# Performance work log

Measured on AMD Instinct MI355X. Metric: run time of the kernel, lower is better.

Reference implementation:

```python
import jax, jax.numpy as jnp
import numpy as np

B, S, D, H, MAX_OBJ, N_IMGS = 256, 256, 256, 4, 50, 32


def setup_inputs() -> dict:
    key = jax.random.key(0)
    ks = jax.random.split(key, 8)
    std = 1.0 / np.sqrt(D)
    mk = lambda k: (jax.random.normal(k, (D, D), jnp.float32) * std)
    return {
        "batch_seq": jax.random.normal(ks[0], (B, S, D), jnp.float32),
        "img_ids": jax.random.randint(ks[1], (B,), 0, N_IMGS, jnp.int32),
        "Wq": mk(ks[2]), "Wk": mk(ks[3]), "Wv": mk(ks[4]), "Wo": mk(ks[5]),
        "bq": jnp.zeros((D,), jnp.float32), "bk": jnp.zeros((D,), jnp.float32),
        "bv": jnp.zeros((D,), jnp.float32), "bo": jnp.zeros((D,), jnp.float32),
        "obj_emb": jax.random.normal(ks[6], (MAX_OBJ, D), jnp.float32) * 0.02,
        "scale": jnp.ones((1,), jnp.float32) * 0.2,
    }


def reference(batch_seq, img_ids, Wq, Wk, Wv, Wo, bq, bk, bv, bo, obj_emb, scale):
    Bn, Sn, Dn = batch_seq.shape
    dh = Dn // H
    idx = jnp.arange(Bn)
    same = img_ids[:, None] == img_ids[None, :]          # (B, B) group membership
    rank = jnp.sum(same & (idx[None, :] < idx[:, None]), axis=1)  # position within group
    gsize = jnp.sum(same, axis=1)                         # group size per item

    # enhanced features: add rank-indexed object embedding (broadcast over seq)
    enh = batch_seq + scale * obj_emb[rank][:, None, :]   # (B, S, D)

    # MHA over the seq dimension, batched over B (eval mode, no dropout)
    q = (enh @ Wq + bq).reshape(Bn, Sn, H, dh)
    k = (enh @ Wk + bk).reshape(Bn, Sn, H, dh)
    v = (enh @ Wv + bv).reshape(Bn, Sn, H, dh)
    scores = jnp.einsum("bqhd,bkhd->bhqk", q, k) / float(np.sqrt(dh))
    attn = jax.nn.softmax(scores, axis=-1)
    ctx = jnp.einsum("bhqk,bkhd->bqhd", attn, v).reshape(Bn, Sn, Dn)
    att_out = ctx @ Wo + bo

    # residual; items in singleton groups are passed through unchanged
    return jnp.where((gsize > 1)[:, None, None], batch_seq + att_out, batch_seq)
```

## Files before the change

### kernel.cpp

```cpp
#include <hip/hip_runtime.h>

typedef __bf16 bf16x8 __attribute__((ext_vector_type(8)));
typedef float f32x4 __attribute__((ext_vector_type(4)));
typedef ushort u16x8 __attribute__((ext_vector_type(8)));

__device__ __forceinline__ float bf2f(ushort u) {
    union { unsigned int i; float f; } v; v.i = ((unsigned int)u) << 16; return v.f;
}
__device__ __forceinline__ ushort f2bf(float f) {
    union { float f; unsigned int i; } v; v.f = f;
    unsigned int i = v.i;
    return (ushort)((i + 0x7FFFu + ((i >> 16) & 1u)) >> 16);
}
__device__ __forceinline__ unsigned int addmul_bf2(unsigned int xs, unsigned int es, float sc) {
    float f0 = bf2f((ushort)(xs & 0xffffu)) + sc * bf2f((ushort)(es & 0xffffu));
    float f1 = bf2f((ushort)(xs >> 16))     + sc * bf2f((ushort)(es >> 16));
    return (unsigned int)f2bf(f0) | (((unsigned int)f2bf(f1)) << 16);
}

__global__ __launch_bounds__(256) void sniff_kernel(
    const unsigned int* __restrict__ bs_words, int* __restrict__ flag)
{
    const int t = threadIdx.x;
    int hit = 0;
    for (int i = 0; i < 64; ++i) {
        unsigned int w = bs_words[t * 64 + i];
        unsigned int e0 = (w >> 7)  & 0xffu;
        unsigned int e1 = (w >> 23) & 0xffu;
        if (e0 > 150u || e1 > 150u) hit = 1;
    }
    __shared__ int s;
    if (t == 0) s = 0;
    __syncthreads();
    if (hit) atomicOr(&s, 1);
    __syncthreads();
    if (t == 0) *flag = s;
}

__global__ __launch_bounds__(256) void prep_kernel(
    const int* __restrict__ flag,
    const void* __restrict__ Wq, const void* __restrict__ Wk,
    const void* __restrict__ Wv, const void* __restrict__ Wo,
    const void* __restrict__ c0, const void* __restrict__ c1,
    const void* __restrict__ c2, const void* __restrict__ c3,
    const void* __restrict__ c4, const void* __restrict__ scale_in,
    int* __restrict__ rank, int* __restrict__ gsize,
    ushort* __restrict__ Wqkv_t, ushort* __restrict__ Wo_t,
    float* __restrict__ bqkv_f, float* __restrict__ bo_f,
    float* __restrict__ scale_f)
{
    const int blk = blockIdx.x;
    const int t = threadIdx.x;
    const bool is_f32 = (*flag != 0);
    if (blk < 256) {
        const int k = blk;
        ushort q, kk, vv, oo;
        if (is_f32) {
            q  = f2bf(((const float*)Wq)[k * 256 + t]);
            kk = f2bf(((const float*)Wk)[k * 256 + t]);
            vv = f2bf(((const float*)Wv)[k * 256 + t]);
            oo = f2bf(((const float*)Wo)[k * 256 + t]);
        } else {
            q  = ((const ushort*)Wq)[k * 256 + t];
            kk = ((const ushort*)Wk)[k * 256 + t];
            vv = ((const ushort*)Wv)[k * 256 + t];
            oo = ((const ushort*)Wo)[k * 256 + t];
        }
        Wqkv_t[(size_t)t * 256 + k]         = q;
        Wqkv_t[(size_t)(256 + t) * 256 + k] = kk;
        Wqkv_t[(size_t)(512 + t) * 256 + k] = vv;
        Wo_t[(size_t)t * 256 + k]           = oo;
    } else {
        const void* cands[5] = {c0, c1, c2, c3, c4};
        __shared__ int cstat[5];
        if (t < 5) cstat[t] = 0;
        __syncthreads();
        #pragma unroll
        for (int c = 0; c < 5; ++c) {
            unsigned int wv = ((const unsigned int*)cands[c])[t];
            int fl = ((wv != 0u) ? 1 : 0) | ((wv >= 32u) ? 2 : 0);
            if (fl) atomicOr(&cstat[c], fl);
        }
        __syncthreads();
        int sel = 0;
        #pragma unroll
        for (int c = 4; c >= 0; --c)
            if (cstat[c] == 1) sel = c;
        const int* ids = (const int*)cands[sel];
        int bp[4];
        { int n = 0;
          #pragma unroll
          for (int c = 0; c < 5; ++c) if (c != sel) bp[n++] = c; }

        const int b = t;
        const int my = ids[b];
        int r = 0, g = 0;
        for (int j = 0; j < 256; ++j) {
            bool same = (ids[j] == my);
            r += (same && (j < b)) ? 1 : 0;
            g += same ? 1 : 0;
        }
        rank[b]  = (r > 49) ? 49 : r;
        gsize[b] = g;

        float vq, vk, vv2, vo2;
        if (is_f32) {
            vq  = ((const float*)cands[bp[0]])[t];
            vk  = ((const float*)cands[bp[1]])[t];
            vv2 = ((const float*)cands[bp[2]])[t];
            vo2 = ((const float*)cands[bp[3]])[t];
            if (t == 0) *scale_f = ((const float*)scale_in)[0];
        } else {
            vq  = bf2f(((const ushort*)cands[bp[0]])[t]);
            vk  = bf2f(((const ushort*)cands[bp[1]])[t]);
            vv2 = bf2f(((const ushort*)cands[bp[2]])[t]);
            vo2 = bf2f(((const ushort*)cands[bp[3]])[t]);
            if (t == 0) *scale_f = bf2f(((const ushort*)scale_in)[0]);
        }
        bqkv_f[t]       = vq;
        bqkv_f[256 + t] = vk;
        bqkv_f[512 + t] = vv2;
        bo_f[t]         = vo2;
    }
}

__global__ __launch_bounds__(256) void enh_kernel(
    const int* __restrict__ flag,
    const void* __restrict__ bs, const void* __restrict__ obj_emb,
    const float* __restrict__ scale_f, const int* __restrict__ rank,
    ushort* __restrict__ enh)
{
    const int idx = blockIdx.x * 256 + threadIdx.x;
    const int e0 = idx * 8;
    const int b = e0 >> 16;
    const int col = e0 & 255;
    const int rk = rank[b];
    const float sc = *scale_f;
    if (*flag != 0) {
        const float* bsf = (const float*)bs + e0;
        const float* ef  = (const float*)obj_emb + rk * 256 + col;
        float4 x0 = *(const float4*)bsf, x1 = *(const float4*)(bsf + 4);
        float4 ev0 = *(const float4*)ef, ev1 = *(const float4*)(ef + 4);
        u16x8 o;
        o[0] = f2bf(x0.x + sc * ev0.x); o[1] = f2bf(x0.y + sc * ev0.y);
        o[2] = f2bf(x0.z + sc * ev0.z); o[3] = f2bf(x0.w + sc * ev0.w);
        o[4] = f2bf(x1.x + sc * ev1.x); o[5] = f2bf(x1.y + sc * ev1.y);
        o[6] = f2bf(x1.z + sc * ev1.z); o[7] = f2bf(x1.w + sc * ev1.w);
        *(u16x8*)(enh + e0) = o;
    } else {
        uint4 x = *(const uint4*)((const ushort*)bs + e0);
        uint4 e = *(const uint4*)((const ushort*)obj_emb + rk * 256 + col);
        uint4 o;
        o.x = addmul_bf2(x.x, e.x, sc);
        o.y = addmul_bf2(x.y, e.y, sc);
        o.z = addmul_bf2(x.z, e.z, sc);
        o.w = addmul_bf2(x.w, e.w, sc);
        *(uint4*)(enh + e0) = o;
    }
}

__global__ __launch_bounds__(256, 2) void qkv_kernel(
    const ushort* __restrict__ enh, const ushort* __restrict__ Wqkv_t,
    const float* __restrict__ bqkv_f,
    ushort* __restrict__ Qg, ushort* __restrict__ Kg, ushort* __restrict__ Vt)
{
    __shared__ __attribute__((aligned(16))) ushort A_lds[64 * 32];
    __shared__ __attribute__((aligned(16))) ushort B_lds[256 * 32];
    __shared__ __attribute__((aligned(16))) ushort Tw[4][64 * 72];

    const int m0 = blockIdx.x * 64;
    const int seg = blockIdx.y;
    const int n0 = seg * 256;
    const int b  = m0 >> 8;
    const int tid = threadIdx.x;
    const int w = tid >> 6, l = tid & 63, quad = l >> 4, l15 = l & 15;

    f32x4 acc[4][4];
    #pragma unroll
    for (int i = 0; i < 4; ++i)
        #pragma unroll
        for (int j = 0; j < 4; ++j) { f32x4 z = {0.f,0.f,0.f,0.f}; acc[i][j] = z; }

    const int arow = tid >> 2, ako = (tid & 3) * 8;
    for (int k0 = 0; k0 < 256; k0 += 32) {
        *(uint4*)&A_lds[arow * 32 + ako] =
            *(const uint4*)(enh + (((size_t)(m0 + arow)) << 8) + k0 + ako);
        #pragma unroll
        for (int i = 0; i < 4; ++i) {
            int f = tid + i * 256;
            int n = f >> 2, ko = (f & 3) * 8;
            *(uint4*)&B_lds[n * 32 + ko] =
                *(const uint4*)(Wqkv_t + (((size_t)(n0 + n)) << 8) + k0 + ko);
        }
        __syncthreads();
        bf16x8 a[4], bb[4];
        #pragma unroll
        for (int mt = 0; mt < 4; ++mt)
            a[mt] = *(const bf16x8*)&A_lds[(mt * 16 + l15) * 32 + quad * 8];
        #pragma unroll
        for (int nt = 0; nt < 4; ++nt)
            bb[nt] = *(const bf16x8*)&B_lds[(w * 64 + nt * 16 + l15) * 32 + quad * 8];
        #pragma unroll
        for (int mt = 0; mt < 4; ++mt)
            #pragma unroll
            for (int nt = 0; nt < 4; ++nt)
                acc[mt][nt] = __builtin_amdgcn_mfma_f32_16x16x32_bf16(
                    a[mt], bb[nt], acc[mt][nt], 0, 0, 0);
        __syncthreads();
    }

    if (seg < 2) {
        const float qs = (seg == 0) ? 0.125f : 1.0f;
        #pragma unroll
        for (int nt = 0; nt < 4; ++nt) {
            const float bias = bqkv_f[seg * 256 + w * 64 + nt * 16 + l15];
            #pragma unroll
            for (int mt = 0; mt < 4; ++mt)
                #pragma unroll
                for (int r = 0; r < 4; ++r)
                    Tw[w][(mt * 16 + quad * 4 + r) * 72 + nt * 16 + l15] =
                        f2bf((acc[mt][nt][r] + bias) * qs);
        }
        ushort* dst = (seg == 0) ? Qg : Kg;
        const size_t bh = (size_t)(b * 4 + w);
        const int sb = m0 & 255;
        #pragma unroll
        for (int i = 0; i < 8; ++i) {
            const int chunk = i * 64 + l;
            const int row = chunk >> 3, dch = chunk & 7;
            u16x8 v = *(const u16x8*)&Tw[w][row * 72 + dch * 8];
            *(u16x8*)(dst + (bh * 256 + sb + row) * 64 + dch * 8) = v;
        }
    } else {
        #pragma unroll
        for (int nt = 0; nt < 4; ++nt) {
            const int n_g = n0 + w * 64 + nt * 16 + l15;
            const int within = n_g & 255;
            const int h = within >> 6, d = within & 63;
            const float bias = bqkv_f[n_g];
            const size_t bh = (size_t)(b * 4 + h);
            #pragma unroll
            for (int mt = 0; mt < 4; ++mt) {
                const int sbase = (m0 & 255) + mt * 16 + quad * 4;
                ushort pk[4];
                #pragma unroll
                for (int r = 0; r < 4; ++r) pk[r] = f2bf(acc[mt][nt][r] + bias);
                *(ushort4*)(Vt + (bh * 64 + d) * 256 + sbase) =
                    make_ushort4(pk[0], pk[1], pk[2], pk[3]);
            }
        }
    }
}

__global__ __launch_bounds__(256, 2) void attn_kernel(
    const ushort* __restrict__ Qg, const ushort* __restrict__ Kg,
    const ushort* __restrict__ Vt, ushort* __restrict__ ctx)
{
    __shared__ __attribute__((aligned(16))) ushort Pl[4][64 * 72];
    const int bh = blockIdx.x;
    const int b = bh >> 2, h = bh & 3;
    const int tid = threadIdx.x;
    const int w = tid >> 6, l = tid & 63, quad = l >> 4, l15 = l & 15;

    const ushort* Qb = Qg + (size_t)bh * 256 * 64;
    const ushort* Kb = Kg + (size_t)bh * 256 * 64;
    const ushort* Vb = Vt + (size_t)bh * 64 * 256;

    bf16x8 qf[4][2];
    #pragma unroll
    for (int mt = 0; mt < 4; ++mt)
        #pragma unroll
        for (int ks = 0; ks < 2; ++ks) {
            int s = w * 64 + mt * 16 + l15;
            qf[mt][ks] = *(const bf16x8*)(Qb + (size_t)s * 64 + ks * 32 + quad * 8);
        }

    f32x4 O[4][4];
    float lsum[4][4];
    #pragma unroll
    for (int mt = 0; mt < 4; ++mt) {
        #pragma unroll
        for (int dt = 0; dt < 4; ++dt) { f32x4 z = {0.f,0.f,0.f,0.f}; O[mt][dt] = z; }
        #pragma unroll
        for (int r = 0; r < 4; ++r) lsum[mt][r] = 0.f;
    }

    for (int c = 0; c < 4; ++c) {
        bf16x8 vf[2][4];
        #pragma unroll
        for (int ks = 0; ks < 2; ++ks)
            #pragma unroll
            for (int dt = 0; dt < 4; ++dt)
                vf[ks][dt] = *(const bf16x8*)(Vb + (size_t)(dt * 16 + l15) * 256 +
                                              c * 64 + ks * 32 + quad * 8);

        f32x4 sacc[4][4];
        #pragma unroll
        for (int mt = 0; mt < 4; ++mt)
            #pragma unroll
            for (int nt = 0; nt < 4; ++nt) { f32x4 z = {0.f,0.f,0.f,0.f}; sacc[mt][nt] = z; }
        #pragma unroll
        for (int ks = 0; ks < 2; ++ks) {
            bf16x8 kf[4];
            #pragma unroll
            for (int nt = 0; nt < 4; ++nt) {
                int key = c * 64 + nt * 16 + l15;
                kf[nt] = *(const bf16x8*)(Kb + (size_t)key * 64 + ks * 32 + quad * 8);
            }
            #pragma unroll
            for (int mt = 0; mt < 4; ++mt)
                #pragma unroll
                for (int nt = 0; nt < 4; ++nt)
                    sacc[mt][nt] = __builtin_amdgcn_mfma_f32_16x16x32_bf16(
                        qf[mt][ks], kf[nt], sacc[mt][nt], 0, 0, 0);
        }

        #pragma unroll
        for (int mt = 0; mt < 4; ++mt)
            #pragma unroll
            for (int nt = 0; nt < 4; ++nt)
                #pragma unroll
                for (int r = 0; r < 4; ++r) {
                    float p = __expf(sacc[mt][nt][r]);
                    lsum[mt][r] += p;
                    Pl[w][(mt * 16 + quad * 4 + r) * 72 + nt * 16 + l15] = f2bf(p);
                }

        #pragma unroll
        for (int ks = 0; ks < 2; ++ks) {
            bf16x8 pf[4];
            #pragma unroll
            for (int mt = 0; mt < 4; ++mt)
                pf[mt] = *(const bf16x8*)&Pl[w][(mt * 16 + l15) * 72 + ks * 32 + quad * 8];
            #pragma unroll
            for (int mt = 0; mt < 4; ++mt)
                #pragma unroll
                for (int dt = 0; dt < 4; ++dt)
                    O[mt][dt] = __builtin_amdgcn_mfma_f32_16x16x32_bf16(
                        pf[mt], vf[ks][dt], O[mt][dt], 0, 0, 0);
        }
    }

    float linv[4][4];
    #pragma unroll
    for (int mt = 0; mt < 4; ++mt)
        #pragma unroll
        for (int r = 0; r < 4; ++r) {
            float v = lsum[mt][r];
            v += __shfl_xor(v, 1);
            v += __shfl_xor(v, 2);
            v += __shfl_xor(v, 4);
            v += __shfl_xor(v, 8);
            linv[mt][r] = 1.0f / v;
        }

    #pragma unroll
    for (int mt = 0; mt < 4; ++mt)
        #pragma unroll
        for (int r = 0; r < 4; ++r) {
            #pragma unroll
            for (int dt = 0; dt < 4; ++dt)
                Pl[w][(mt * 16 + quad * 4 + r) * 72 + dt * 16 + l15] =
                    f2bf(O[mt][dt][r] * linv[mt][r]);
        }
    #pragma unroll
    for (int i = 0; i < 8; ++i) {
        const int chunk = i * 64 + l;
        const int row = chunk >> 3, dch = chunk & 7;
        u16x8 v = *(const u16x8*)&Pl[w][row * 72 + dch * 8];
        *(u16x8*)(ctx + ((size_t)(b * 256 + w * 64 + row)) * 256 + h * 64 + dch * 8) = v;
    }
}

__global__ __launch_bounds__(256, 2) void out_kernel(
    const int* __restrict__ flag,
    const ushort* __restrict__ ctx, const ushort* __restrict__ Wo_t,
    const float* __restrict__ bo_f, const void* __restrict__ bs,
    const int* __restrict__ gsize, void* __restrict__ outv)
{
    __shared__ __attribute__((aligned(16))) ushort A_lds[64 * 32];
    __shared__ __attribute__((aligned(16))) ushort B_lds[256 * 32];
    __shared__ __attribute__((aligned(16))) float  Tf[4][16 * 68];

    const int m0 = blockIdx.x * 64;
    const int tid = threadIdx.x;
    const int w = tid >> 6, l = tid & 63, quad = l >> 4, l15 = l & 15;
    const int b = m0 >> 8;
    const bool pass = (gsize[b] <= 1);
    const bool is_f32 = (*flag != 0);

    f32x4 acc[4][4];
    #pragma unroll
    for (int i = 0; i < 4; ++i)
        #pragma unroll
        for (int j = 0; j < 4; ++j) { f32x4 z = {0.f,0.f,0.f,0.f}; acc[i][j] = z; }

    const int arow = tid >> 2, ako = (tid & 3) * 8;
    for (int k0 = 0; k0 < 256; k0 += 32) {
        *(uint4*)&A_lds[arow * 32 + ako] =
            *(const uint4*)(ctx + (((size_t)(m0 + arow)) << 8) + k0 + ako);
        #pragma unroll
        for (int i = 0; i < 4; ++i) {
            int f = tid + i * 256;
            int n = f >> 2, ko = (f & 3) * 8;
            *(uint4*)&B_lds[n * 32 + ko] =
                *(const uint4*)(Wo_t + (((size_t)n) << 8) + k0 + ko);
        }
        __syncthreads();
        bf16x8 a[4], bb[4];
        #pragma unroll
        for (int mt = 0; mt < 4; ++mt)
            a[mt] = *(const bf16x8*)&A_lds[(mt * 16 + l15) * 32 + quad * 8];
        #pragma unroll
        for (int nt = 0; nt < 4; ++nt)
            bb[nt] = *(const bf16x8*)&B_lds[(w * 64 + nt * 16 + l15) * 32 + quad * 8];
        #pragma unroll
        for (int mt = 0; mt < 4; ++mt)
            #pragma unroll
            for (int nt = 0; nt < 4; ++nt)
                acc[mt][nt] = __builtin_amdgcn_mfma_f32_16x16x32_bf16(
                    a[mt], bb[nt], acc[mt][nt], 0, 0, 0);
        __syncthreads();
    }

    for (int mt = 0; mt < 4; ++mt) {
        #pragma unroll
        for (int nt = 0; nt < 4; ++nt) {
            const float bias = bo_f[w * 64 + nt * 16 + l15];
            #pragma unroll
            for (int r = 0; r < 4; ++r)
                Tf[w][(quad * 4 + r) * 68 + nt * 16 + l15] = acc[mt][nt][r] + bias;
        }
        #pragma unroll
        for (int i = 0; i < 4; ++i) {
            const int chunk = i * 64 + l;
            const int row = chunk >> 4, c4 = chunk & 15;
            f32x4 v = *(const f32x4*)&Tf[w][row * 68 + c4 * 4];
            const int token = m0 + mt * 16 + row;
            const size_t idx = (((size_t)token) << 8) + w * 64 + c4 * 4;
            if (is_f32) {
                float4 base = *(const float4*)((const float*)bs + idx);
                float4 o;
                o.x = pass ? base.x : base.x + v[0];
                o.y = pass ? base.y : base.y + v[1];
                o.z = pass ? base.z : base.z + v[2];
                o.w = pass ? base.w : base.w + v[3];
                *(float4*)((float*)outv + idx) = o;
            } else {
                ushort4 b4 = *(const ushort4*)((const ushort*)bs + idx);
                ushort4 o;
                o.x = pass ? b4.x : f2bf(bf2f(b4.x) + v[0]);
                o.y = pass ? b4.y : f2bf(bf2f(b4.y) + v[1]);
                o.z = pass ? b4.z : f2bf(bf2f(b4.z) + v[2]);
                o.w = pass ? b4.w : f2bf(bf2f(b4.w) + v[3]);
                *(ushort4*)((ushort*)outv + idx) = o;
            }
        }
    }
}

extern "C" void kernel_launch(void* const* d_in, const int* in_sizes, int n_in,
                              void* d_out, int out_size, void* d_ws, size_t ws_size,
                              hipStream_t stream)
{
    int bs_i = -1, obj_i = -1, sc_i = -1;
    int w_i[4] = {2, 3, 4, 5}; int nw = 0;
    int c_i[5] = {1, 6, 7, 8, 9}; int nc = 0;
    for (int i = 0; i < n_in; ++i) {
        int s = in_sizes[i];
        if      (s == 16777216) bs_i = i;
        else if (s == 65536)  { if (nw < 4) w_i[nw] = i; ++nw; }
        else if (s == 12800)    obj_i = i;
        else if (s == 1)        sc_i = i;
        else if (s == 256)    { if (nc < 5) c_i[nc] = i; ++nc; }
    }
    if (bs_i < 0 || obj_i < 0 || sc_i < 0 || nw != 4 || nc != 5) {
        bs_i = 0; obj_i = 10; sc_i = 11;
        w_i[0] = 2; w_i[1] = 3; w_i[2] = 4; w_i[3] = 5;
        c_i[0] = 1; c_i[1] = 6; c_i[2] = 7; c_i[3] = 8; c_i[4] = 9;
    }
    const void* bs    = d_in[bs_i];
    const void* Wq    = d_in[w_i[0]];
    const void* Wk    = d_in[w_i[1]];
    const void* Wv    = d_in[w_i[2]];
    const void* Wo    = d_in[w_i[3]];
    const void* obj   = d_in[obj_i];
    const void* scale = d_in[sc_i];

    char* ws = (char*)d_ws;
    int*    flag    = (int*)ws;
    int*    rank    = (int*)(ws + 1024);
    int*    gsize   = (int*)(ws + 2048);
    float*  scale_f = (float*)(ws + 3072);
    float*  bqkv_f  = (float*)(ws + 4096);
    float*  bo_f    = (float*)(ws + 8192);
    ushort* Wqkv_t  = (ushort*)(ws + 16384);
    ushort* Wo_t    = (ushort*)(ws + 409600);
    ushort* enh     = (ushort*)(ws + ((size_t)1  << 20));
    ushort* ctx     = (ushort*)(ws + ((size_t)33 << 20));
    ushort* Vt      = (ushort*)(ws + ((size_t)65 << 20));

    ushort* Qg = (ushort*)d_out;
    ushort* Kg = Qg + 16777216;

    hipLaunchKernelGGL(sniff_kernel, dim3(1), dim3(256), 0, stream,
                       (const unsigned int*)bs, flag);
    hipLaunchKernelGGL(prep_kernel, dim3(257), dim3(256), 0, stream,
                       flag, Wq, Wk, Wv, Wo,
                       d_in[c_i[0]], d_in[c_i[1]], d_in[c_i[2]],
                       d_in[c_i[3]], d_in[c_i[4]], scale,
                       rank, gsize, Wqkv_t, Wo_t, bqkv_f, bo_f, scale_f);
    hipLaunchKernelGGL(enh_kernel, dim3(8192), dim3(256), 0, stream,
                       flag, bs, obj, scale_f, rank, enh);
    hipLaunchKernelGGL(qkv_kernel, dim3(1024, 3), dim3(256), 0, stream,
                       enh, Wqkv_t, bqkv_f, Qg, Kg, Vt);
    hipLaunchKernelGGL(attn_kernel, dim3(1024), dim3(256), 0, stream,
                       Qg, Kg, Vt, ctx);
    hipLaunchKernelGGL(out_kernel, dim3(1024), dim3(256), 0, stream,
                       flag, ctx, Wo_t, bo_f, bs, gsize, d_out);
}
```

Baseline: 281.8 us.

## Fuse enhancement into QKV GEMM and enlarge GEMM M-tiles to 128

Removes the separate enh_kernel. The QKV GEMM now reads batch_seq and obj_emb directly, applies the scaled embedding add and bf16 conversion while staging A tiles into LDS, which avoids writing and re-reading a 32MB intermediate. Both the QKV and output GEMMs move from 64-row to 128-row M tiles, doubling per-block accumulators so each weight tile loaded into LDS is reused across more rows. The costs are higher register pressure (32 accumulator tiles per wave), fewer blocks, and, for the f32 input path, recomputing the conversion in each of the three column-segment blocks.

```diff
diff --git a/kernel.cpp b/kernel.cpp
--- a/kernel.cpp
+++ b/kernel.cpp
@@ -124,67 +124,65 @@
     }
 }
 
-__global__ __launch_bounds__(256) void enh_kernel(
+__global__ __launch_bounds__(256, 2) void qkv_kernel(
     const int* __restrict__ flag,
     const void* __restrict__ bs, const void* __restrict__ obj_emb,
     const float* __restrict__ scale_f, const int* __restrict__ rank,
-    ushort* __restrict__ enh)
-{
-    const int idx = blockIdx.x * 256 + threadIdx.x;
-    const int e0 = idx * 8;
-    const int b = e0 >> 16;
-    const int col = e0 & 255;
-    const int rk = rank[b];
-    const float sc = *scale_f;
-    if (*flag != 0) {
-        const float* bsf = (const float*)bs + e0;
-        const float* ef  = (const float*)obj_emb + rk * 256 + col;
-        float4 x0 = *(const float4*)bsf, x1 = *(const float4*)(bsf + 4);
-        float4 ev0 = *(const float4*)ef, ev1 = *(const float4*)(ef + 4);
-        u16x8 o;
-        o[0] = f2bf(x0.x + sc * ev0.x); o[1] = f2bf(x0.y + sc * ev0.y);
-        o[2] = f2bf(x0.z + sc * ev0.z); o[3] = f2bf(x0.w + sc * ev0.w);
-        o[4] = f2bf(x1.x + sc * ev1.x); o[5] = f2bf(x1.y + sc * ev1.y);
-        o[6] = f2bf(x1.z + sc * ev1.z); o[7] = f2bf(x1.w + sc * ev1.w);
-        *(u16x8*)(enh + e0) = o;
-    } else {
-        uint4 x = *(const uint4*)((const ushort*)bs + e0);
-        uint4 e = *(const uint4*)((const ushort*)obj_emb + rk * 256 + col);
-        uint4 o;
-        o.x = addmul_bf2(x.x, e.x, sc);
-        o.y = addmul_bf2(x.y, e.y, sc);
-        o.z = addmul_bf2(x.z, e.z, sc);
-        o.w = addmul_bf2(x.w, e.w, sc);
-        *(uint4*)(enh + e0) = o;
-    }
-}
-
-__global__ __launch_bounds__(256, 2) void qkv_kernel(
-    const ushort* __restrict__ enh, const ushort* __restrict__ Wqkv_t,
-    const float* __restrict__ bqkv_f,
+    const ushort* __restrict__ Wqkv_t, const float* __restrict__ bqkv_f,
     ushort* __restrict__ Qg, ushort* __restrict__ Kg, ushort* __restrict__ Vt)
 {
-    __shared__ __attribute__((aligned(16))) ushort A_lds[64 * 32];
+    __shared__ __attribute__((aligned(16))) ushort A_lds[128 * 32];
     __shared__ __attribute__((aligned(16))) ushort B_lds[256 * 32];
     __shared__ __attribute__((aligned(16))) ushort Tw[4][64 * 72];
 
-    const int m0 = blockIdx.x * 64;
+    const int m0 = blockIdx.x * 128;
     const int seg = blockIdx.y;
     const int n0 = seg * 256;
     const int b  = m0 >> 8;
     const int tid = threadIdx.x;
     const int w = tid >> 6, l = tid & 63, quad = l >> 4, l15 = l & 15;
-
-    f32x4 acc[4][4];
-    #pragma unroll
-    for (int i = 0; i < 4; ++i)
+    const bool is_f32 = (*flag != 0);
+    const float sc = *scale_f;
+    const int rk = rank[b];
+
+    f32x4 acc[8][4];
+    #pragma unroll
+    for (int i = 0; i < 8; ++i)
         #pragma unroll
         for (int j = 0; j < 4; ++j) { f32x4 z = {0.f,0.f,0.f,0.f}; acc[i][j] = z; }
 
     const int arow = tid >> 2, ako = (tid & 3) * 8;
     for (int k0 = 0; k0 < 256; k0 += 32) {
-        *(uint4*)&A_lds[arow * 32 + ako] =
-            *(const uint4*)(enh + (((size_t)(m0 + arow)) << 8) + k0 + ako);
+        #pragma unroll
+        for (int p = 0; p < 2; ++p) {
+            const int row = p * 64 + arow;
+            const size_t off = (((size_t)(m0 + row)) << 8) + k0 + ako;
+            if (is_f32) {
+                const float* bsf = (const float*)bs;
+                const float* ef  = (const float*)obj_emb + rk * 256 + k0 + ako;
+                float4 x0 = *(const float4*)(bsf + off);
+                float4 x1 = *(const float4*)(bsf + off + 4);
+                float4 e0 = *(const float4*)(ef);
+                float4 e1 = *(const float4*)(ef + 4);
+                u16x8 o;
+                o[0] = f2bf(x0.x + sc * e0.x); o[1] = f2bf(x0.y + sc * e0.y);
+                o[2] = f2bf(x0.z + sc * e0.z); o[3] = f2bf(x0.w + sc * e0.w);
+                o[4] = f2bf(x1.x + sc * e1.x); o[5] = f2bf(x1.y + sc * e1.y);
+                o[6] = f2bf(x1.z + sc * e1.z); o[7] = f2bf(x1.w + sc * e1.w);
+                *(u16x8*)&A_lds[row * 32 + ako] = o;
+            } else {
+                const ushort* b16 = (const ushort*)bs;
+                const ushort* ef  = (const ushort*)obj_emb + rk * 256 + k0 + ako;
+                uint4 x = *(const uint4*)(b16 + off);
+                uint4 e = *(const uint4*)ef;
+                uint4 o;
+                o.x = addmul_bf2(x.x, e.x, sc);
+                o.y = addmul_bf2(x.y, e.y, sc);
+                o.z = addmul_bf2(x.z, e.z, sc);
+                o.w = addmul_bf2(x.w, e.w, sc);
+                *(uint4*)&A_lds[row * 32 + ako] = o;
+            }
+        }
         #pragma unroll
         for (int i = 0; i < 4; ++i) {
             int f = tid + i * 256;
@@ -193,15 +191,15 @@
                 *(const uint4*)(Wqkv_t + (((size_t)(n0 + n)) << 8) + k0 + ko);
         }
         __syncthreads();
-        bf16x8 a[4], bb[4];
-        #pragma unroll
-        for (int mt = 0; mt < 4; ++mt)
+        bf16x8 a[8], bb[4];
+        #pragma unroll
+        for (int mt = 0; mt < 8; ++mt)
             a[mt] = *(const bf16x8*)&A_lds[(mt * 16 + l15) * 32 + quad * 8];
         #pragma unroll
         for (int nt = 0; nt < 4; ++nt)
             bb[nt] = *(const bf16x8*)&B_lds[(w * 64 + nt * 16 + l15) * 32 + quad * 8];
         #pragma unroll
-        for (int mt = 0; mt < 4; ++mt)
+        for (int mt = 0; mt < 8; ++mt)
             #pragma unroll
             for (int nt = 0; nt < 4; ++nt)
                 acc[mt][nt] = __builtin_amdgcn_mfma_f32_16x16x32_bf16(
@@ -211,36 +209,37 @@
 
     if (seg < 2) {
         const float qs = (seg == 0) ? 0.125f : 1.0f;
-        #pragma unroll
-        for (int nt = 0; nt < 4; ++nt) {
-            const float bias = bqkv_f[seg * 256 + w * 64 + nt * 16 + l15];
-            #pragma unroll
-            for (int mt = 0; mt < 4; ++mt)
-                #pragma unroll
-                for (int r = 0; r < 4; ++r)
-                    Tw[w][(mt * 16 + quad * 4 + r) * 72 + nt * 16 + l15] =
-                        f2bf((acc[mt][nt][r] + bias) * qs);
-        }
         ushort* dst = (seg == 0) ? Qg : Kg;
         const size_t bh = (size_t)(b * 4 + w);
-        const int sb = m0 & 255;
-        #pragma unroll
-        for (int i = 0; i < 8; ++i) {
-            const int chunk = i * 64 + l;
-            const int row = chunk >> 3, dch = chunk & 7;
-            u16x8 v = *(const u16x8*)&Tw[w][row * 72 + dch * 8];
-            *(u16x8*)(dst + (bh * 256 + sb + row) * 64 + dch * 8) = v;
+        #pragma unroll
+        for (int half = 0; half < 2; ++half) {
+            #pragma unroll
+            for (int nt = 0; nt < 4; ++nt) {
+                const float bias = bqkv_f[seg * 256 + w * 64 + nt * 16 + l15];
+                #pragma unroll
+                for (int mt2 = 0; mt2 < 4; ++mt2)
+                    #pragma unroll
+                    for (int r = 0; r < 4; ++r)
+                        Tw[w][(mt2 * 16 + quad * 4 + r) * 72 + nt * 16 + l15] =
+                            f2bf((acc[half * 4 + mt2][nt][r] + bias) * qs);
+            }
+            const int sb = (m0 & 255) + half * 64;
+            #pragma unroll
+            for (int i = 0; i < 8; ++i) {
+                const int chunk = i * 64 + l;
+                const int row = chunk >> 3, dch = chunk & 7;
+                u16x8 v = *(const u16x8*)&Tw[w][row * 72 + dch * 8];
+                *(u16x8*)(dst + (bh * 256 + sb + row) * 64 + dch * 8) = v;
+            }
         }
     } else {
+        const size_t bh = (size_t)(b * 4 + w);
         #pragma unroll
         for (int nt = 0; nt < 4; ++nt) {
-            const int n_g = n0 + w * 64 + nt * 16 + l15;
-            const int within = n_g & 255;
-            const int h = within >> 6, d = within & 63;
-            const float bias = bqkv_f[n_g];
-            const size_t bh = (size_t)(b * 4 + h);
-            #pragma unroll
-            for (int mt = 0; mt < 4; ++mt) {
+            const int d = nt * 16 + l15;
+            const float bias = bqkv_f[512 + w * 64 + d];
+            #pragma unroll
+            for (int mt = 0; mt < 8; ++mt) {
                 const int sbase = (m0 & 255) + mt * 16 + quad * 4;
                 ushort pk[4];
                 #pragma unroll
@@ -378,27 +377,31 @@
     const float* __restrict__ bo_f, const void* __restrict__ bs,
     const int* __restrict__ gsize, void* __restrict__ outv)
 {
-    __shared__ __attribute__((aligned(16))) ushort A_lds[64 * 32];
+    __shared__ __attribute__((aligned(16))) ushort A_lds[128 * 32];
     __shared__ __attribute__((aligned(16))) ushort B_lds[256 * 32];
     __shared__ __attribute__((aligned(16))) float  Tf[4][16 * 68];
 
-    const int m0 = blockIdx.x * 64;
+    const int m0 = blockIdx.x * 128;
     const int tid = threadIdx.x;
     const int w = tid >> 6, l = tid & 63, quad = l >> 4, l15 = l & 15;
     const int b = m0 >> 8;
     const bool pass = (gsize[b] <= 1);
     const bool is_f32 = (*flag != 0);
 
-    f32x4 acc[4][4];
-    #pragma unroll
-    for (int i = 0; i < 4; ++i)
+    f32x4 acc[8][4];
+    #pragma unroll
+    for (int i = 0; i < 8; ++i)
         #pragma unroll
         for (int j = 0; j < 4; ++j) { f32x4 z = {0.f,0.f,0.f,0.f}; acc[i][j] = z; }
 
     const int arow = tid >> 2, ako = (tid & 3) * 8;
     for (int k0 = 0; k0 < 256; k0 += 32) {
-        *(uint4*)&A_lds[arow * 32 + ako] =
-            *(const uint4*)(ctx + (((size_t)(m0 + arow)) << 8) + k0 + ako);
+        #pragma unroll
+        for (int p = 0; p < 2; ++p) {
+            const int row = p * 64 + arow;
+            *(uint4*)&A_lds[row * 32 + ako] =
+                *(const uint4*)(ctx + (((size_t)(m0 + row)) << 8) + k0 + ako);
+        }
         #pragma unroll
         for (int i = 0; i < 4; ++i) {
             int f = tid + i * 256;
@@ -407,15 +410,15 @@
                 *(const uint4*)(Wo_t + (((size_t)n) << 8) + k0 + ko);
         }
         __syncthreads();
-        bf16x8 a[4], bb[4];
-        #pragma unroll
-        for (int mt = 0; mt < 4; ++mt)
+        bf16x8 a[8], bb[4];
+        #pragma unroll
+        for (int mt = 0; mt < 8; ++mt)
             a[mt] = *(const bf16x8*)&A_lds[(mt * 16 + l15) * 32 + quad * 8];
         #pragma unroll
         for (int nt = 0; nt < 4; ++nt)
             bb[nt] = *(const bf16x8*)&B_lds[(w * 64 + nt * 16 + l15) * 32 + quad * 8];
         #pragma unroll
-        for (int mt = 0; mt < 4; ++mt)
+        for (int mt = 0; mt < 8; ++mt)
             #pragma unroll
             for (int nt = 0; nt < 4; ++nt)
                 acc[mt][nt] = __builtin_amdgcn_mfma_f32_16x16x32_bf16(
@@ -423,7 +426,7 @@
         __syncthreads();
     }
 
-    for (int mt = 0; mt < 4; ++mt) {
+    for (int mt = 0; mt < 8; ++mt) {
         #pragma unroll
         for (int nt = 0; nt < 4; ++nt) {
             const float bias = bo_f[w * 64 + nt * 16 + l15];
@@ -496,7 +499,6 @@
     float*  bo_f    = (float*)(ws + 8192);
     ushort* Wqkv_t  = (ushort*)(ws + 16384);
     ushort* Wo_t    = (ushort*)(ws + 409600);
-    ushort* enh     = (ushort*)(ws + ((size_t)1  << 20));
     ushort* ctx     = (ushort*)(ws + ((size_t)33 << 20));
     ushort* Vt      = (ushort*)(ws + ((size_t)65 << 20));
 
@@ -510,12 +512,11 @@
                        d_in[c_i[0]], d_in[c_i[1]], d_in[c_i[2]],
                        d_in[c_i[3]], d_in[c_i[4]], scale,
                        rank, gsize, Wqkv_t, Wo_t, bqkv_f, bo_f, scale_f);
-    hipLaunchKernelGGL(enh_kernel, dim3(8192), dim3(256), 0, stream,
-                       flag, bs, obj, scale_f, rank, enh);
-    hipLaunchKernelGGL(qkv_kernel, dim3(1024, 3), dim3(256), 0, stream,
-                       enh, Wqkv_t, bqkv_f, Qg, Kg, Vt);
+    hipLaunchKernelGGL(qkv_kernel, dim3(512, 3), dim3(256), 0, stream,
+                       flag, bs, obj, scale_f, rank, Wqkv_t, bqkv_f,
+                       Qg, Kg, Vt);
     hipLaunchKernelGGL(attn_kernel, dim3(1024), dim3(256), 0, stream,
                        Qg, Kg, Vt, ctx);
-    hipLaunchKernelGGL(out_kernel, dim3(1024), dim3(256), 0, stream,
+    hipLaunchKernelGGL(out_kernel, dim3(512), dim3(256), 0, stream,
                        flag, ctx, Wo_t, bo_f, bs, gsize, d_out);
 }
```

Result: slower. 400.8 us (+42.2%).
